# Kernel optimization log

Hardware: AMD Instinct MI355X
Metric: run time of the kernel (lower is better)

Reference implementation:

```python
import jax, jax.numpy as jnp
import numpy as np

N_NODES = 100000
N_EDGES = 1600000
IN_C, HID_C, OUT_C = 128, 128, 64


def setup_inputs() -> dict:
    key = jax.random.key(0)
    ks = jax.random.split(key, 9)
    features = jax.random.normal(ks[0], (N_NODES, IN_C), dtype=jnp.float32)
    src = jax.random.randint(ks[1], (N_EDGES,), 0, N_NODES, dtype=jnp.int32)
    dst = jax.random.randint(ks[2], (N_EDGES,), 0, N_NODES, dtype=jnp.int32)
    def glorot(k, fan_in, fan_out):
        lim = float(np.sqrt(6.0 / (fan_in + fan_out)))
        return jax.random.uniform(k, (fan_in, fan_out), jnp.float32, -lim, lim)
    return {
        "features": features, "src": src, "dst": dst,
        "W1": glorot(ks[3], IN_C, HID_C), "b1": jnp.zeros((HID_C,), jnp.float32),
        "W2": glorot(ks[4], HID_C, HID_C), "b2": jnp.zeros((HID_C,), jnp.float32),
        "W3": glorot(ks[5], HID_C, OUT_C), "b3": jnp.zeros((OUT_C,), jnp.float32),
    }


def _graph_conv(x, src, dst, W, b, inv_sqrt_out, inv_sqrt_in):
    # DGL GraphConv, norm='both': h = D_in^{-1/2} A D_out^{-1/2} (x W) + b
    h = (x * inv_sqrt_out[:, None]) @ W            # [N, out]
    agg = jax.ops.segment_sum(h[src], dst, num_segments=N_NODES)
    return agg * inv_sqrt_in[:, None] + b


def reference(features, src, dst, W1, b1, W2, b2, W3, b3):
    ones = jnp.ones((N_EDGES,), jnp.float32)
    deg_out = jnp.clip(jax.ops.segment_sum(ones, src, num_segments=N_NODES), 1.0)
    deg_in = jnp.clip(jax.ops.segment_sum(ones, dst, num_segments=N_NODES), 1.0)
    iso, isi = deg_out ** -0.5, deg_in ** -0.5
    x = jax.nn.relu(_graph_conv(features, src, dst, W1, b1, iso, isi))
    x = jax.nn.relu(_graph_conv(x, src, dst, W2, b2, iso, isi))
    x = _graph_conv(x, src, dst, W3, b3, iso, isi)
    return jax.nn.log_softmax(x, axis=1)
```

## Files before the change

kernel.cpp:

```cpp
#include <hip/hip_runtime.h>
#include <hip/hip_bf16.h>

#define IN_C 128
#define HID_C 128
#define OUT_C 64

typedef unsigned short u16;
typedef unsigned int   u32;
typedef __attribute__((ext_vector_type(8))) short short8;
typedef __attribute__((ext_vector_type(4))) float f32x4;
typedef __attribute__((ext_vector_type(2))) float f32x2;

__device__ __forceinline__ u16 bf16_bits(float x) {
    __hip_bfloat16 h = __float2bfloat16(x);
    return *(u16*)&h;
}
__device__ __forceinline__ void split_hi_lo(float a, u16& hi, u16& lo) {
    __hip_bfloat16 h = __float2bfloat16(a);
    float hf = __bfloat162float(h);
    __hip_bfloat16 l = __float2bfloat16(a - hf);
    hi = *(u16*)&h; lo = *(u16*)&l;
}
__device__ __forceinline__ void pk_acc(f32x2& acc, u32 v) {
    f32x2 val;
    val.x = __uint_as_float(v << 16);
    val.y = __uint_as_float(v & 0xffff0000u);
    asm("v_pk_add_f32 %0, %0, %1" : "+v"(acc) : "v"(val));
}


__global__ void zero_kernel(int* __restrict__ p, int n) {
    int i = blockIdx.x * blockDim.x + threadIdx.x;
    if (i < n) p[i] = 0;
}

__global__ void degree_src(const int* __restrict__ src, int* __restrict__ cnt, int E) {
    for (int i = blockIdx.x * blockDim.x + threadIdx.x; i < E; i += gridDim.x * blockDim.x)
        atomicAdd(&cnt[src[i]], 1);
}


__global__ __launch_bounds__(256)
void part_hist(const int* __restrict__ dst, int* __restrict__ bh,
               int E, int K, int NB) {
    const int b = blockIdx.x;
    extern __shared__ int lh[];
    for (int i = threadIdx.x; i < K; i += 256) lh[i] = 0;
    __syncthreads();
    const int lo = (int)((long long)E * b / NB);
    const int hi = (int)((long long)E * (b + 1) / NB);
    for (int i = lo + threadIdx.x; i < hi; i += 256)
        atomicAdd(&lh[__builtin_nontemporal_load(&dst[i]) >> 8], 1);
    __syncthreads();
    for (int k = threadIdx.x; k < K; k += 256)
        bh[k * NB + b] = lh[k];
}

__global__ __launch_bounds__(256)
void part_scatter(const int* __restrict__ src, const int* __restrict__ dst,
                  const int* __restrict__ ofs, u32* __restrict__ pairs,
                  int E, int K, int NB) {
    const int b = blockIdx.x;
    extern __shared__ int lcur[];
    for (int k = threadIdx.x; k < K; k += 256) lcur[k] = ofs[k * NB + b];
    __syncthreads();
    const int lo = (int)((long long)E * b / NB);
    const int hi = (int)((long long)E * (b + 1) / NB);
    for (int i = lo + threadIdx.x; i < hi; i += 256) {
        int d = __builtin_nontemporal_load(&dst[i]);
        int s = __builtin_nontemporal_load(&src[i]);
        int p = atomicAdd(&lcur[d >> 8], 1);
        pairs[p] = ((u32)s << 8) | (u32)(d & 255);
    }
}

__global__ __launch_bounds__(256)
void bucket_count_fill(const u32* __restrict__ pairs, const int* __restrict__ OFS,
                       const int* __restrict__ cnt_out,
                       int* __restrict__ csr, int* __restrict__ row_start,
                       int* __restrict__ row_end, float* __restrict__ iso,
                       float* __restrict__ isi, int N, int NB, int K, int E) {
    const int k = blockIdx.x, t = threadIdx.x;
    __shared__ int lc[256];
    __shared__ int lpre[256];
    lc[t] = 0;
    __syncthreads();
    const int s0 = OFS[k * NB];
    const int s1 = (k == K - 1) ? E : OFS[(k + 1) * NB];
    for (int i = s0 + t; i < s1; i += 256)
        atomicAdd(&lc[pairs[i] & 255], 1);
    __syncthreads();
    const int c  = lc[t];
    const int cp = (c + 3) & ~3;
    lpre[t] = cp;
    __syncthreads();
    for (int off = 1; off < 256; off <<= 1) {
        int v = (t >= off) ? lpre[t - off] : 0;
        __syncthreads();
        lpre[t] += v;
        __syncthreads();
    }
    const int start = s0 + k * 768 + lpre[t] - cp;
    const int myend = start + cp;
    const int node = k * 256 + t;
    if (node < N) {
        row_start[node] = start;
        row_end[node]   = myend;
        int di = c < 1 ? 1 : c;
        int co = cnt_out[node];
        int dd = co < 1 ? 1 : co;
        isi[node] = rsqrtf((float)di);
        iso[node] = rsqrtf((float)dd);
    }
    __syncthreads();
    lc[t] = start;
    __syncthreads();
    for (int i = s0 + t; i < s1; i += 256) {
        u32 pr = pairs[i];
        int p = atomicAdd(&lc[pr & 255], 1);
        csr[p] = (int)(pr >> 8);
    }
    __syncthreads();
    if (node < N) {
        for (int q = lc[t]; q < myend; ++q) csr[q] = N;
    }
}


__global__ __launch_bounds__(256)
void scan_pass1(const int* __restrict__ in, int* __restrict__ blocksum, int M) {
    const int b = blockIdx.x, t = threadIdx.x;
    const int base = b * 1024 + t * 4;
    int s = 0;
#pragma unroll
    for (int j = 0; j < 4; ++j) {
        int idx = base + j;
        if (idx < M) s += in[idx];
    }
#pragma unroll
    for (int off = 32; off >= 1; off >>= 1) s += __shfl_xor(s, off);
    __shared__ int wsum[4];
    if ((t & 63) == 0) wsum[t >> 6] = s;
    __syncthreads();
    if (t == 0) blocksum[b] = wsum[0] + wsum[1] + wsum[2] + wsum[3];
}

__global__ __launch_bounds__(1024)
void scan_g2(int* __restrict__ a, int nb) {
    __shared__ int s[1024];
    const int t = threadIdx.x;
    int v = (t < nb) ? a[t] : 0;
    s[t] = v;
    __syncthreads();
    for (int off = 1; off < 1024; off <<= 1) {
        int x = (t >= off) ? s[t - off] : 0;
        __syncthreads();
        s[t] += x;
        __syncthreads();
    }
    if (t < nb) a[t] = s[t] - v;
}

__global__ __launch_bounds__(256)
void scan_g3(const int* __restrict__ in, const int* __restrict__ blockoff,
             int* __restrict__ out, int M) {
    __shared__ int ssum[256];
    const int b = blockIdx.x, t = threadIdx.x;
    const int base = b * 1024 + t * 4;
    int c[4];
#pragma unroll
    for (int j = 0; j < 4; ++j) {
        int idx = base + j;
        c[j] = (idx < M) ? in[idx] : 0;
    }
    const int tot = c[0] + c[1] + c[2] + c[3];
    ssum[t] = tot;
    __syncthreads();
    for (int off = 1; off < 256; off <<= 1) {
        int v = (t >= off) ? ssum[t - off] : 0;
        __syncthreads();
        ssum[t] += v;
        __syncthreads();
    }
    int run = blockoff[b] + ssum[t] - tot;
#pragma unroll
    for (int j = 0; j < 4; ++j) {
        int idx = base + j;
        if (idx < M) { out[idx] = run; run += c[j]; }
    }
}


__global__ __launch_bounds__(128)
void wt_prep_all(const float* __restrict__ W1, const float* __restrict__ W2,
                 const float* __restrict__ W3, u16* __restrict__ Wt1,
                 u16* __restrict__ Wt2, u16* __restrict__ Wt3) {
    const int b = blockIdx.x, k = threadIdx.x;
    if (b < 128)       Wt1[b * 128 + k] = bf16_bits(W1[k * 128 + b]);
    else if (b < 256)  { int c = b - 128; Wt2[c * 128 + k] = bf16_bits(W2[k * 128 + c]); }
    else               { int c = b - 256; Wt3[c * 128 + k] = bf16_bits(W3[k * 64 + c]); }
}


template <int C>
__device__ __forceinline__
void mfma_store2(const u16* sAh, const u16* sAl, const u16* __restrict__ Wt,
                 u16* __restrict__ H, int row0, int N, int t) {
    constexpr int NT = C / 16;
    const int wid = t >> 6, lane = t & 63;
    const int r0 = wid * 16;
    const int arow = r0 + (lane & 15);
    const int kb = (lane >> 4) * 8;

    f32x4 acc[NT];
#pragma unroll
    for (int i = 0; i < NT; ++i) acc[i] = (f32x4){0.f, 0.f, 0.f, 0.f};

    const u16* wbase = Wt + (size_t)(lane & 15) * 128 + kb;

#pragma unroll
    for (int kk = 0; kk < 4; ++kk) {
        short8 ah = *(const short8*)(&sAh[arow * 136 + kk * 32 + kb]);
        short8 al = *(const short8*)(&sAl[arow * 136 + kk * 32 + kb]);
#pragma unroll
        for (int ct = 0; ct < NT; ++ct) {
            short8 bf = *(const short8*)(wbase + ct * 16 * 128 + kk * 32);
            acc[ct] = __builtin_amdgcn_mfma_f32_16x16x32_bf16(ah, bf, acc[ct], 0, 0, 0);
            acc[ct] = __builtin_amdgcn_mfma_f32_16x16x32_bf16(al, bf, acc[ct], 0, 0, 0);
        }
    }

    const int rbase = row0 + r0 + (lane >> 4) * 4;
#pragma unroll
    for (int ct = 0; ct < NT; ++ct) {
        int gcol = ct * 16 + (lane & 15);
#pragma unroll
        for (int r = 0; r < 4; ++r) {
            int grow = rbase + r;
            if (grow < N) H[(size_t)grow * C + gcol] = bf16_bits(acc[ct][r]);
        }
    }
}

template <int C>
__device__ __forceinline__
void mfma_store1(const u16* sA, const u16* __restrict__ Wt,
                 u16* __restrict__ H, int row0, int N, int t) {
    constexpr int NT = C / 16;
    const int wid = t >> 6, lane = t & 63;
    const int r0 = wid * 16;
    const int arow = r0 + (lane & 15);
    const int kb = (lane >> 4) * 8;

    f32x4 acc[NT];
#pragma unroll
    for (int i = 0; i < NT; ++i) acc[i] = (f32x4){0.f, 0.f, 0.f, 0.f};

    const u16* wbase = Wt + (size_t)(lane & 15) * 128 + kb;

#pragma unroll
    for (int kk = 0; kk < 4; ++kk) {
        short8 a = *(const short8*)(&sA[arow * 136 + kk * 32 + kb]);
#pragma unroll
        for (int ct = 0; ct < NT; ++ct) {
            short8 bf = *(const short8*)(wbase + ct * 16 * 128 + kk * 32);
            acc[ct] = __builtin_amdgcn_mfma_f32_16x16x32_bf16(a, bf, acc[ct], 0, 0, 0);
        }
    }

    const int rbase = row0 + r0 + (lane >> 4) * 4;
#pragma unroll
    for (int ct = 0; ct < NT; ++ct) {
        int gcol = ct * 16 + (lane & 15);
#pragma unroll
        for (int r = 0; r < 4; ++r) {
            int grow = rbase + r;
            if (grow < N) H[(size_t)grow * C + gcol] = bf16_bits(acc[ct][r]);
        }
    }
}


__global__ __launch_bounds__(256)
void gemm1_fused(const float* __restrict__ X, const float* __restrict__ iso,
                 const u16* __restrict__ Wt, u16* __restrict__ H, int N) {
    __shared__ u16 sAh[64 * 136];
    __shared__ u16 sAl[64 * 136];
    const int t = threadIdx.x;
    const int row0 = blockIdx.x * 64;

    if (blockIdx.x == 0 && t < 64) ((u32*)H)[(size_t)N * 64 + t] = 0;

    for (int i = t; i < 2048; i += 256) {
        int r = i >> 5, kv = (i & 31) << 2;
        int gr = row0 + r;
        if (gr >= N) gr = N - 1;
        float s = iso[gr];
        float4 x = *(const float4*)(X + (size_t)gr * 128 + kv);
        u16 h0, l0, h1, l1, h2, l2, h3, l3;
        split_hi_lo(x.x * s, h0, l0);
        split_hi_lo(x.y * s, h1, l1);
        split_hi_lo(x.z * s, h2, l2);
        split_hi_lo(x.w * s, h3, l3);
        uint2 hp = make_uint2((u32)h0 | ((u32)h1 << 16), (u32)h2 | ((u32)h3 << 16));
        uint2 lp = make_uint2((u32)l0 | ((u32)l1 << 16), (u32)l2 | ((u32)l3 << 16));
        *(uint2*)(&sAh[r * 136 + kv]) = hp;
        *(uint2*)(&sAl[r * 136 + kv]) = lp;
    }
    __syncthreads();
    mfma_store2<128>(sAh, sAl, Wt, H, row0, N, t);
}


template <int C>
__global__ __launch_bounds__(256)
void gemm_mfma(const u16* __restrict__ A,
               const u16* __restrict__ Wt, u16* __restrict__ H, int N) {
    __shared__ u16 sA[64 * 136];
    const int t = threadIdx.x;
    const int row0 = blockIdx.x * 64;

    if (blockIdx.x == 0 && t < C / 2) ((u32*)H)[(size_t)N * (C / 2) + t] = 0;

    for (int c = t; c < 1024; c += 256) {
        int r = c >> 4, kc = c & 15;
        int gr = row0 + r;
        if (gr >= N) gr = N - 1;
        *(uint4*)(&sA[r * 136 + kc * 8]) = *(const uint4*)(A + (size_t)gr * 128 + kc * 8);
    }
    __syncthreads();
    mfma_store1<C>(sA, Wt, H, row0, N, t);
}


__device__ __forceinline__
void gather128w(const u16* __restrict__ Hin, const int* __restrict__ csr,
                int rs, int re, int lane, f32x2* acc) {
    const int sub = lane >> 4;
    const int cb  = (lane & 15) * 8;
    int e = rs;
    while (e < re) {
        int nloc = re - e;
        if (nloc > 64) nloc = 64;
        int idx = (lane < nloc) ? __builtin_nontemporal_load(&csr[e + lane]) : 0;
        int j = 0;
        for (; j + 16 <= nloc; j += 16) {
            int r0 = __shfl(idx, j + sub);
            int r1 = __shfl(idx, j + 4 + sub);
            int r2 = __shfl(idx, j + 8 + sub);
            int r3 = __shfl(idx, j + 12 + sub);
            uint4 v0 = *(const uint4*)(Hin + (size_t)r0 * 128 + cb);
            uint4 v1 = *(const uint4*)(Hin + (size_t)r1 * 128 + cb);
            uint4 v2 = *(const uint4*)(Hin + (size_t)r2 * 128 + cb);
            uint4 v3 = *(const uint4*)(Hin + (size_t)r3 * 128 + cb);
            pk_acc(acc[0], v0.x); pk_acc(acc[1], v0.y); pk_acc(acc[2], v0.z); pk_acc(acc[3], v0.w);
            pk_acc(acc[0], v1.x); pk_acc(acc[1], v1.y); pk_acc(acc[2], v1.z); pk_acc(acc[3], v1.w);
            pk_acc(acc[0], v2.x); pk_acc(acc[1], v2.y); pk_acc(acc[2], v2.z); pk_acc(acc[3], v2.w);
            pk_acc(acc[0], v3.x); pk_acc(acc[1], v3.y); pk_acc(acc[2], v3.z); pk_acc(acc[3], v3.w);
        }
        for (; j < nloc; j += 4) {
            int r0 = __shfl(idx, j + sub);
            uint4 v0 = *(const uint4*)(Hin + (size_t)r0 * 128 + cb);
            pk_acc(acc[0], v0.x); pk_acc(acc[1], v0.y); pk_acc(acc[2], v0.z); pk_acc(acc[3], v0.w);
        }
        e += nloc;
    }
}


__global__ __launch_bounds__(256)
void agg_relu(const u16* __restrict__ H, const int* __restrict__ row_start,
              const int* __restrict__ row_end,
              const int* __restrict__ csr_src, const float* __restrict__ isi,
              const float* __restrict__ iso, const float* __restrict__ bias,
              u16* __restrict__ A, int N) {
    const int wid  = (int)((blockIdx.x * (size_t)blockDim.x + threadIdx.x) >> 6);
    const int lane = threadIdx.x & 63;
    if (wid >= N) return;
    const int rs = row_start[wid];
    const int re = row_end[wid];

    f32x2 acc[4];
#pragma unroll
    for (int i = 0; i < 4; ++i) { acc[i].x = 0.f; acc[i].y = 0.f; }
    gather128w(H, csr_src, rs, re, lane, acc);

#pragma unroll
    for (int i = 0; i < 4; ++i) {
        acc[i].x += __shfl_xor(acc[i].x, 16); acc[i].y += __shfl_xor(acc[i].y, 16);
        acc[i].x += __shfl_xor(acc[i].x, 32); acc[i].y += __shfl_xor(acc[i].y, 32);
    }

    if (lane < 16) {
        const float sc = isi[wid], so = iso[wid];
        float4 ba = *(const float4*)(bias + lane * 8);
        float4 bb = *(const float4*)(bias + lane * 8 + 4);
        float o[8];
        o[0] = acc[0].x * sc + ba.x; o[1] = acc[0].y * sc + ba.y;
        o[2] = acc[1].x * sc + ba.z; o[3] = acc[1].y * sc + ba.w;
        o[4] = acc[2].x * sc + bb.x; o[5] = acc[2].y * sc + bb.y;
        o[6] = acc[3].x * sc + bb.z; o[7] = acc[3].y * sc + bb.w;
        u32 hp[4];
#pragma unroll
        for (int i = 0; i < 4; ++i) {
            u16 h0 = bf16_bits(fmaxf(o[2 * i], 0.f) * so);
            u16 h1 = bf16_bits(fmaxf(o[2 * i + 1], 0.f) * so);
            hp[i] = (u32)h0 | ((u32)h1 << 16);
        }
        *(uint4*)(A + (size_t)wid * 128 + lane * 8) = *(uint4*)hp;
    }
}


__global__ __launch_bounds__(256)
void agg_final(const u16* __restrict__ H, const int* __restrict__ row_start,
               const int* __restrict__ row_end,
               const int* __restrict__ csr_src, const float* __restrict__ isi,
               const float* __restrict__ bias, float* __restrict__ Out, int N) {
    const int wid  = (int)((blockIdx.x * (size_t)blockDim.x + threadIdx.x) >> 6);
    const int lane = threadIdx.x & 63;
    if (wid >= N) return;
    const int rs = row_start[wid];
    const int re = row_end[wid];
    const int sub = lane >> 4;
    const int cb  = (lane & 15) * 4;

    f32x2 a0, a1;
    a0.x = a0.y = a1.x = a1.y = 0.f;
    int e = rs;
    while (e < re) {
        int nloc = re - e;
        if (nloc > 64) nloc = 64;
        int idx = (lane < nloc) ? __builtin_nontemporal_load(&csr_src[e + lane]) : 0;
        int j = 0;
        for (; j + 16 <= nloc; j += 16) {
            int r0 = __shfl(idx, j + sub);
            int r1 = __shfl(idx, j + 4 + sub);
            int r2 = __shfl(idx, j + 8 + sub);
            int r3 = __shfl(idx, j + 12 + sub);
            uint2 v0 = *(const uint2*)(H + (size_t)r0 * 64 + cb);
            uint2 v1 = *(const uint2*)(H + (size_t)r1 * 64 + cb);
            uint2 v2 = *(const uint2*)(H + (size_t)r2 * 64 + cb);
            uint2 v3 = *(const uint2*)(H + (size_t)r3 * 64 + cb);
            pk_acc(a0, v0.x); pk_acc(a1, v0.y);
            pk_acc(a0, v1.x); pk_acc(a1, v1.y);
            pk_acc(a0, v2.x); pk_acc(a1, v2.y);
            pk_acc(a0, v3.x); pk_acc(a1, v3.y);
        }
        for (; j < nloc; j += 4) {
            int r0 = __shfl(idx, j + sub);
            uint2 v0 = *(const uint2*)(H + (size_t)r0 * 64 + cb);
            pk_acc(a0, v0.x); pk_acc(a1, v0.y);
        }
        e += nloc;
    }

    a0.x += __shfl_xor(a0.x, 16); a0.y += __shfl_xor(a0.y, 16);
    a0.x += __shfl_xor(a0.x, 32); a0.y += __shfl_xor(a0.y, 32);
    a1.x += __shfl_xor(a1.x, 16); a1.y += __shfl_xor(a1.y, 16);
    a1.x += __shfl_xor(a1.x, 32); a1.y += __shfl_xor(a1.y, 32);

    const float sc = isi[wid];
    float4 b4 = *(const float4*)(bias + (lane & 15) * 4);
    float v0 = a0.x * sc + b4.x;
    float v1 = a0.y * sc + b4.y;
    float v2 = a1.x * sc + b4.z;
    float v3 = a1.y * sc + b4.w;
    float m = fmaxf(fmaxf(v0, v1), fmaxf(v2, v3));
#pragma unroll
    for (int off = 8; off >= 1; off >>= 1) m = fmaxf(m, __shfl_xor(m, off));
    float ss = expf(v0 - m) + expf(v1 - m) + expf(v2 - m) + expf(v3 - m);
#pragma unroll
    for (int off = 8; off >= 1; off >>= 1) ss += __shfl_xor(ss, off);
    float lg = m + logf(ss);
    if (lane < 16) {
        float4 o = make_float4(v0 - lg, v1 - lg, v2 - lg, v3 - lg);
        *(float4*)(Out + (size_t)wid * 64 + lane * 4) = o;
    }
}


extern "C" void kernel_launch(void* const* d_in, const int* in_sizes, int n_in,
                              void* d_out, int out_size, void* d_ws, size_t ws_size,
                              hipStream_t stream) {
    const float* features = (const float*)d_in[0];
    const int*   src      = (const int*)d_in[1];
    const int*   dst      = (const int*)d_in[2];
    const float* W1       = (const float*)d_in[3];
    const float* b1       = (const float*)d_in[4];
    const float* W2       = (const float*)d_in[5];
    const float* b2       = (const float*)d_in[6];
    const float* W3       = (const float*)d_in[7];
    const float* b3       = (const float*)d_in[8];
    float*       out      = (float*)d_out;

    const int N  = in_sizes[0] / IN_C;
    const int E  = in_sizes[1];
    const int K  = (N + 255) >> 8;
    const int NB = 256;
    const int M  = K * NB;
    const int nbe = (M + 1023) / 1024;

    char* ws = (char*)d_ws;
    const size_t SLOT = 400128;
    int*   cnt_out   = (int*)(ws + 0 * SLOT);
    int*   row_end   = (int*)(ws + 1 * SLOT);
    int*   row_start = (int*)(ws + 2 * SLOT);
    float* iso       = (float*)(ws + 3 * SLOT);
    float* isi       = (float*)(ws + 4 * SLOT);
    int*   eblocksum = (int*)(ws + 5 * SLOT);
    int*   csr       = (int*)(ws + 6 * SLOT);
    char*  p         = ws + 6 * SLOT + 8000128;
    int*   BH        = (int*)p;
    int*   OFS       = (int*)(p + 500224);
    u32*   pairs     = (u32*)(p + 1000448);
    u16*   Hb        = (u16*)(p + 7401472);
    u16*   Ab        = (u16*)(p + 33001728);
    u16*   Wt1       = (u16*)(p + 58601728);
    u16*   Wt2       = Wt1 + 128 * 128;
    u16*   Wt3       = Wt2 + 128 * 128;

    const size_t ldsK = (size_t)K * sizeof(int);

    zero_kernel<<<(N + 255) / 256, 256, 0, stream>>>(cnt_out, N);
    degree_src<<<1024, 256, 0, stream>>>(src, cnt_out, E);
    part_hist<<<NB, 256, ldsK, stream>>>(dst, BH, E, K, NB);
    scan_pass1<<<nbe, 256, 0, stream>>>(BH, eblocksum, M);
    scan_g2<<<1, 1024, 0, stream>>>(eblocksum, nbe);
    scan_g3<<<nbe, 256, 0, stream>>>(BH, eblocksum, OFS, M);
    part_scatter<<<NB, 256, ldsK, stream>>>(src, dst, OFS, pairs, E, K, NB);
    bucket_count_fill<<<K, 256, 0, stream>>>(pairs, OFS, cnt_out, csr, row_start,
                                             row_end, iso, isi, N, NB, K, E);

    wt_prep_all<<<320, 128, 0, stream>>>(W1, W2, W3, Wt1, Wt2, Wt3);

    const int gblocks = (N + 63) / 64;
    const int ablocks = (int)(((size_t)N * 64 + 255) / 256);

    gemm1_fused<<<gblocks, 256, 0, stream>>>(features, iso, Wt1, Hb, N);
    agg_relu<<<ablocks, 256, 0, stream>>>(Hb, row_start, row_end, csr, isi, iso, b1, Ab, N);
    gemm_mfma<128><<<gblocks, 256, 0, stream>>>(Ab, Wt2, Hb, N);
    agg_relu<<<ablocks, 256, 0, stream>>>(Hb, row_start, row_end, csr, isi, iso, b2, Ab, N);
    gemm_mfma<64><<<gblocks, 256, 0, stream>>>(Ab, Wt3, Hb, N);
    agg_final<<<ablocks, 256, 0, stream>>>(Hb, row_start, row_end, csr, isi, b3, out, N);
}
```

Before: 391.2 us.

## Compute out-degrees via bucketed LDS partition instead of global atomics

Removes the zero and global-atomic out-degree kernels. The partition histogram and scatter now also bucket edges by source node, and a new per-bucket kernel counts source degrees in shared memory to produce iso. This avoids contended global atomics but doubles the scan length and the pair-buffer writes, and adds one more pass over the pairs.

```diff
diff --git a/kernel.cpp b/kernel.cpp
--- a/kernel.cpp
+++ b/kernel.cpp
@@ -29,57 +29,72 @@
 }
 
 
-__global__ void zero_kernel(int* __restrict__ p, int n) {
-    int i = blockIdx.x * blockDim.x + threadIdx.x;
-    if (i < n) p[i] = 0;
-}
-
-__global__ void degree_src(const int* __restrict__ src, int* __restrict__ cnt, int E) {
-    for (int i = blockIdx.x * blockDim.x + threadIdx.x; i < E; i += gridDim.x * blockDim.x)
-        atomicAdd(&cnt[src[i]], 1);
-}
-
-
-__global__ __launch_bounds__(256)
-void part_hist(const int* __restrict__ dst, int* __restrict__ bh,
-               int E, int K, int NB) {
+__global__ __launch_bounds__(256)
+void part_hist2(const int* __restrict__ src, const int* __restrict__ dst,
+                int* __restrict__ bh, int E, int K, int NB) {
     const int b = blockIdx.x;
     extern __shared__ int lh[];
-    for (int i = threadIdx.x; i < K; i += 256) lh[i] = 0;
-    __syncthreads();
-    const int lo = (int)((long long)E * b / NB);
-    const int hi = (int)((long long)E * (b + 1) / NB);
-    for (int i = lo + threadIdx.x; i < hi; i += 256)
-        atomicAdd(&lh[__builtin_nontemporal_load(&dst[i]) >> 8], 1);
-    __syncthreads();
-    for (int k = threadIdx.x; k < K; k += 256)
-        bh[k * NB + b] = lh[k];
-}
-
-__global__ __launch_bounds__(256)
-void part_scatter(const int* __restrict__ src, const int* __restrict__ dst,
-                  const int* __restrict__ ofs, u32* __restrict__ pairs,
-                  int E, int K, int NB) {
-    const int b = blockIdx.x;
-    extern __shared__ int lcur[];
-    for (int k = threadIdx.x; k < K; k += 256) lcur[k] = ofs[k * NB + b];
+    for (int i = threadIdx.x; i < 2 * K; i += 256) lh[i] = 0;
     __syncthreads();
     const int lo = (int)((long long)E * b / NB);
     const int hi = (int)((long long)E * (b + 1) / NB);
     for (int i = lo + threadIdx.x; i < hi; i += 256) {
         int d = __builtin_nontemporal_load(&dst[i]);
         int s = __builtin_nontemporal_load(&src[i]);
-        int p = atomicAdd(&lcur[d >> 8], 1);
-        pairs[p] = ((u32)s << 8) | (u32)(d & 255);
+        atomicAdd(&lh[d >> 8], 1);
+        atomicAdd(&lh[K + (s >> 8)], 1);
+    }
+    __syncthreads();
+    for (int k = threadIdx.x; k < K; k += 256) {
+        bh[k * NB + b]       = lh[k];
+        bh[(K + k) * NB + b] = lh[K + k];
+    }
+}
+
+__global__ __launch_bounds__(256)
+void part_scatter2(const int* __restrict__ src, const int* __restrict__ dst,
+                   const int* __restrict__ ofs, u32* __restrict__ pairs,
+                   int E, int K, int NB) {
+    const int b = blockIdx.x;
+    extern __shared__ int lcur[];
+    for (int k = threadIdx.x; k < 2 * K; k += 256) lcur[k] = ofs[k * NB + b];
+    __syncthreads();
+    const int lo = (int)((long long)E * b / NB);
+    const int hi = (int)((long long)E * (b + 1) / NB);
+    for (int i = lo + threadIdx.x; i < hi; i += 256) {
+        int d = __builtin_nontemporal_load(&dst[i]);
+        int s = __builtin_nontemporal_load(&src[i]);
+        int p1 = atomicAdd(&lcur[d >> 8], 1);
+        pairs[p1] = ((u32)s << 8) | (u32)(d & 255);
+        int p2 = atomicAdd(&lcur[K + (s >> 8)], 1);
+        pairs[p2] = (u32)s;
+    }
+}
+
+__global__ __launch_bounds__(256)
+void bucket_count_src(const u32* __restrict__ pairs, const int* __restrict__ OFS,
+                      float* __restrict__ iso, int N, int NB, int K, int E) {
+    const int k = blockIdx.x, t = threadIdx.x;
+    __shared__ int lc[256];
+    lc[t] = 0;
+    __syncthreads();
+    const int s0 = OFS[(K + k) * NB];
+    const int s1 = (k == K - 1) ? 2 * E : OFS[(K + k + 1) * NB];
+    for (int i = s0 + t; i < s1; i += 256)
+        atomicAdd(&lc[pairs[i] & 255], 1);
+    __syncthreads();
+    const int node = k * 256 + t;
+    if (node < N) {
+        int c = lc[t];
+        iso[node] = rsqrtf((float)(c < 1 ? 1 : c));
     }
 }
 
 __global__ __launch_bounds__(256)
 void bucket_count_fill(const u32* __restrict__ pairs, const int* __restrict__ OFS,
-                       const int* __restrict__ cnt_out,
                        int* __restrict__ csr, int* __restrict__ row_start,
-                       int* __restrict__ row_end, float* __restrict__ iso,
-                       float* __restrict__ isi, int N, int NB, int K, int E) {
+                       int* __restrict__ row_end, float* __restrict__ isi,
+                       int N, int NB, int K, int E) {
     const int k = blockIdx.x, t = threadIdx.x;
     __shared__ int lc[256];
     __shared__ int lpre[256];
@@ -106,11 +121,7 @@
     if (node < N) {
         row_start[node] = start;
         row_end[node]   = myend;
-        int di = c < 1 ? 1 : c;
-        int co = cnt_out[node];
-        int dd = co < 1 ? 1 : co;
-        isi[node] = rsqrtf((float)di);
-        iso[node] = rsqrtf((float)dd);
+        isi[node] = rsqrtf((float)(c < 1 ? 1 : c));
     }
     __syncthreads();
     lc[t] = start;
@@ -498,12 +509,11 @@
     const int E  = in_sizes[1];
     const int K  = (N + 255) >> 8;
     const int NB = 256;
-    const int M  = K * NB;
+    const int M  = 2 * K * NB;
     const int nbe = (M + 1023) / 1024;
 
     char* ws = (char*)d_ws;
     const size_t SLOT = 400128;
-    int*   cnt_out   = (int*)(ws + 0 * SLOT);
     int*   row_end   = (int*)(ws + 1 * SLOT);
     int*   row_start = (int*)(ws + 2 * SLOT);
     float* iso       = (float*)(ws + 3 * SLOT);
@@ -512,25 +522,24 @@
     int*   csr       = (int*)(ws + 6 * SLOT);
     char*  p         = ws + 6 * SLOT + 8000128;
     int*   BH        = (int*)p;
-    int*   OFS       = (int*)(p + 500224);
-    u32*   pairs     = (u32*)(p + 1000448);
-    u16*   Hb        = (u16*)(p + 7401472);
-    u16*   Ab        = (u16*)(p + 33001728);
-    u16*   Wt1       = (u16*)(p + 58601728);
+    int*   OFS       = (int*)(p + 1000448);
+    u32*   pairs     = (u32*)(p + 2000896);
+    u16*   Hb        = (u16*)(p + 14801408);
+    u16*   Ab        = (u16*)(p + 40401664);
+    u16*   Wt1       = (u16*)(p + 66001664);
     u16*   Wt2       = Wt1 + 128 * 128;
     u16*   Wt3       = Wt2 + 128 * 128;
 
-    const size_t ldsK = (size_t)K * sizeof(int);
-
-    zero_kernel<<<(N + 255) / 256, 256, 0, stream>>>(cnt_out, N);
-    degree_src<<<1024, 256, 0, stream>>>(src, cnt_out, E);
-    part_hist<<<NB, 256, ldsK, stream>>>(dst, BH, E, K, NB);
+    const size_t ldsK2 = (size_t)(2 * K) * sizeof(int);
+
+    part_hist2<<<NB, 256, ldsK2, stream>>>(src, dst, BH, E, K, NB);
     scan_pass1<<<nbe, 256, 0, stream>>>(BH, eblocksum, M);
     scan_g2<<<1, 1024, 0, stream>>>(eblocksum, nbe);
     scan_g3<<<nbe, 256, 0, stream>>>(BH, eblocksum, OFS, M);
-    part_scatter<<<NB, 256, ldsK, stream>>>(src, dst, OFS, pairs, E, K, NB);
-    bucket_count_fill<<<K, 256, 0, stream>>>(pairs, OFS, cnt_out, csr, row_start,
-                                             row_end, iso, isi, N, NB, K, E);
+    part_scatter2<<<NB, 256, ldsK2, stream>>>(src, dst, OFS, pairs, E, K, NB);
+    bucket_count_src<<<K, 256, 0, stream>>>(pairs, OFS, iso, N, NB, K, E);
+    bucket_count_fill<<<K, 256, 0, stream>>>(pairs, OFS, csr, row_start,
+                                             row_end, isi, N, NB, K, E);
 
     wt_prep_all<<<320, 128, 0, stream>>>(W1, W2, W3, Wt1, Wt2, Wt3);
 
```

Measured after the change: 354.9 us. -9.3%, faster.
